# Kernel tuning notes

Measured on AMD Instinct MI355X. Metric: run time of the kernel, lower is better.

## Reference

```python
import jax, jax.numpy as jnp
import numpy as np

N_NODES = 50000
N_EDGES = 800000
IN_DIM = 128
HID_DIM = 256
OUT_DIM = 2


def setup_inputs() -> dict:
    key = jax.random.key(0)
    k = jax.random.split(key, 8)
    x = jax.random.normal(k[0], (N_NODES, IN_DIM), dtype=jnp.float32)
    edge_index = jax.random.randint(k[1], (2, N_EDGES), 0, N_NODES, dtype=jnp.int64)
    # Linear params (PyTorch-style fan-in scaling)
    W1 = jax.random.normal(k[2], (IN_DIM, HID_DIM), dtype=jnp.float32) / np.sqrt(IN_DIM)
    b1 = jnp.zeros((HID_DIM,), dtype=jnp.float32)
    W2 = jax.random.normal(k[3], (HID_DIM, OUT_DIM), dtype=jnp.float32) / np.sqrt(HID_DIM)
    b2 = jnp.zeros((OUT_DIM,), dtype=jnp.float32)
    # learnable GIN epsilons (init 0, as in PyG GINConv train_eps)
    eps1 = jnp.zeros((), dtype=jnp.float32)
    eps2 = jnp.zeros((), dtype=jnp.float32)
    return {"x": x, "edge_index": edge_index, "W1": W1, "b1": b1,
            "W2": W2, "b2": b2, "eps1": eps1, "eps2": eps2}


def _gin_conv(h, src, dst, num_nodes, eps, W, b):
    # aggregate: sum of neighbor features (scatter-add over edges)
    agg = jax.ops.segment_sum(h[src], dst, num_segments=num_nodes)  # [N, D]
    return ((1.0 + eps) * h + agg) @ W + b


def reference(x, edge_index, W1, b1, W2, b2, eps1, eps2):
    src, dst = edge_index[0], edge_index[1]
    n = x.shape[0]
    h = _gin_conv(x, src, dst, n, eps1, W1, b1)   # [N, HID]
    h = jax.nn.relu(h)
    out = _gin_conv(h, src, dst, n, eps2, W2, b2)  # [N, OUT]
    return out
```

## Files before the change

kernel.cpp:

```cpp
#include <hip/hip_runtime.h>

#define N_NODES 50000
#define N_EDGES 800000
#define IN_DIM 128
#define HID_DIM 256
#define OUT_DIM 2
#define CAP 64
#define NBKT 196
#define BCAP 6144
#define CHUNK 4096
#define POISON 0xAAAAAAAAu

typedef __attribute__((ext_vector_type(8))) short bh8;
typedef __attribute__((ext_vector_type(4))) float f4;
typedef __attribute__((ext_vector_type(4))) unsigned u4;

__device__ inline unsigned bf16rne(float f) {
    unsigned u = __float_as_uint(f);
    return (u + 0x7fffu + ((u >> 16) & 1u)) >> 16;
}
__device__ inline unsigned pack2(float lo, float hi) {
    return (bf16rne(hi) << 16) | bf16rne(lo);
}

__global__ __launch_bounds__(256) void k_prep_bin(
    const float* __restrict__ x, const float* __restrict__ W1,
    const int* __restrict__ ei,
    unsigned* __restrict__ xb, unsigned* __restrict__ W1p,
    unsigned* __restrict__ ccur, unsigned* __restrict__ coarse)
{
    __shared__ unsigned stage[CHUNK];
    __shared__ int hist[256], base[256], gpos[256], cur2[256];
    __shared__ int s_red[4];
    const int tid = threadIdx.x, lane = tid & 63, wv = tid >> 6;
    const int gtid = blockIdx.x * 256 + tid;
    const int gsz  = gridDim.x * 256;

    for (int i = gtid; i < 800000; i += gsz) {
        float4 a = ((const float4*)x)[2 * i];
        float4 b = ((const float4*)x)[2 * i + 1];
        u4 w;
        w[0] = pack2(a.x, a.y);
        w[1] = pack2(a.z, a.w);
        w[2] = pack2(b.x, b.y);
        w[3] = pack2(b.z, b.w);
        ((u4*)xb)[i] = w;
    }
    if (gtid < 16384) {
        int j = gtid;
        int d = j & 3, l = (j >> 2) & 63, s = (j >> 8) & 3, t = j >> 10;
        int k = 32 * s + 8 * (l >> 4) + 2 * d;
        int n = 16 * t + (l & 15);
        W1p[j] = (bf16rne(W1[(size_t)(k + 1) * HID_DIM + n]) << 16)
               |  bf16rne(W1[(size_t)k * HID_DIM + n]);
    }
    const int bid = blockIdx.x;
    if (bid >= NBKT) return;
    const int ebase = bid * CHUNK;
    const int ecnt  = min(CHUNK, N_EDGES - ebase);

    hist[tid] = 0;
    __syncthreads();
    int myd[16], mys[16];
#pragma unroll
    for (int r = 0; r < 16; r++) {
        int li = r * 256 + tid;
        if (li < ecnt) {
            int e = ebase + li;
            myd[r] = ei[N_EDGES + e];
            mys[r] = ei[e];
            atomicAdd(&hist[myd[r] >> 8], 1);
        } else myd[r] = -1;
    }
    __syncthreads();
    {
        int v = hist[tid], s = v;
#pragma unroll
        for (int off = 1; off < 64; off <<= 1) {
            int t = __shfl_up(s, off, 64);
            if (lane >= off) s += t;
        }
        if (lane == 63) s_red[wv] = s;
        __syncthreads();
        int wexcl = 0;
        for (int w = 0; w < wv; w++) wexcl += s_red[w];
        base[tid] = wexcl + s - v;
        cur2[tid] = 0;
        __syncthreads();
    }
    if (tid < NBKT && hist[tid] > 0) {
        atomicCAS(&ccur[tid], POISON, 0u);
        gpos[tid] = (int)atomicAdd(&ccur[tid], (unsigned)hist[tid]);
    }
    __syncthreads();
#pragma unroll
    for (int r = 0; r < 16; r++) {
        if (myd[r] >= 0) {
            int b = myd[r] >> 8;
            int pos = atomicAdd(&cur2[b], 1);
            stage[base[b] + pos] = ((unsigned)myd[r] << 16) | (unsigned)mys[r];
        }
    }
    __syncthreads();
    for (int i = tid; i < ecnt; i += 256) {
        unsigned rec = stage[i];
        int b = (int)(rec >> 24);
        int idx = gpos[b] + (i - base[b]);
        if (idx < BCAP) coarse[(size_t)b * BCAP + idx] = rec;
    }
}

__global__ __launch_bounds__(1024) void k_fine(
    const unsigned* __restrict__ ccur, const unsigned* __restrict__ coarse,
    int* __restrict__ slots, int* __restrict__ cnt)
{
    __shared__ int cur[256];
    const int tid = threadIdx.x, bid = blockIdx.x;
    if (tid < 256) cur[tid] = 0;
    __syncthreads();
    const int cb = min((int)ccur[bid], BCAP);
    unsigned recs[6];
#pragma unroll
    for (int r = 0; r < 6; r++) {
        int i = tid + r * 1024;
        if (i < cb) recs[r] = coarse[(size_t)bid * BCAP + i];
    }
#pragma unroll
    for (int r = 0; r < 6; r++) {
        int i = tid + r * 1024;
        if (i < cb) {
            unsigned rec = recs[r];
            int dst = (int)(rec >> 16);
            int src = (int)(rec & 0xffffu);
            int pos = atomicAdd(&cur[dst & 255], 1);
            if (pos < CAP) slots[(size_t)dst * CAP + pos] = src;
        }
    }
    __syncthreads();
    if (tid < 256) {
        int node = bid * 256 + tid;
        if (node < N_NODES) cnt[node] = min(cur[tid], CAP);
    }
}

__global__ __launch_bounds__(256, 4) void k_gin1(
    const unsigned* __restrict__ xb,
    const int* __restrict__ cnt, const int* __restrict__ slots,
    const unsigned* __restrict__ W1p, const float* __restrict__ b1,
    const float* __restrict__ W2, const float* __restrict__ b2,
    const float* __restrict__ eps1p, const float* __restrict__ eps2p,
    float* __restrict__ p, float* __restrict__ out)
{
    __shared__ __attribute__((aligned(16))) unsigned z[16 * 68];
    __shared__ float2 pp[64];
    const int tid = threadIdx.x, lane = tid & 63, wv = tid >> 6;
    const int node0 = blockIdx.x * 16;
    const int sub = lane & 15;
    const int grp = lane >> 4;
    const int node = node0 + 4 * wv + grp;
    const float e1 = 1.0f + eps1p[0];
    const u4* __restrict__ xb4 = (const u4*)xb;

    const int cn = min(cnt[node], CAP);
    const int4* srow = (const int4*)(slots + (size_t)node * CAP);
    int4 sg0 = srow[0], sg1 = srow[1], sg2 = srow[2], sg3 = srow[3];

    u4 us = xb4[(unsigned)(node * 16 + sub)];

    int sq[16];
    sq[0]=sg0.x;  sq[1]=sg0.y;  sq[2]=sg0.z;  sq[3]=sg0.w;
    sq[4]=sg1.x;  sq[5]=sg1.y;  sq[6]=sg1.z;  sq[7]=sg1.w;
    sq[8]=sg2.x;  sq[9]=sg2.y;  sq[10]=sg2.z; sq[11]=sg2.w;
    sq[12]=sg3.x; sq[13]=sg3.y; sq[14]=sg3.z; sq[15]=sg3.w;
#pragma unroll
    for (int g = 0; g < 16; g++) sq[g] = (g < cn) ? sq[g] : 0;

    u4 u[16];
#pragma unroll
    for (int g = 0; g < 16; g++)
        u[g] = xb4[(unsigned)(sq[g] * 16 + sub)];

    float ax[8];
#pragma unroll
    for (int k = 0; k < 8; k++) ax[k] = 0.f;
#pragma unroll
    for (int g = 0; g < 16; g++) {
        if (g < cn) {
#pragma unroll
            for (int k2 = 0; k2 < 4; k2++) {
                unsigned w = u[g][k2];
                ax[2 * k2]     += __uint_as_float(w << 16);
                ax[2 * k2 + 1] += __uint_as_float(w & 0xffff0000u);
            }
        }
    }
    int j0 = 16;
    while (__any(cn > j0)) {
        const int4* trow = (const int4*)(slots + (size_t)node * CAP + j0);
        int4 t0 = trow[0], t1 = trow[1], t2 = trow[2], t3 = trow[3];
        int tq[16];
        tq[0]=t0.x;  tq[1]=t0.y;  tq[2]=t0.z;  tq[3]=t0.w;
        tq[4]=t1.x;  tq[5]=t1.y;  tq[6]=t1.z;  tq[7]=t1.w;
        tq[8]=t2.x;  tq[9]=t2.y;  tq[10]=t2.z; tq[11]=t2.w;
        tq[12]=t3.x; tq[13]=t3.y; tq[14]=t3.z; tq[15]=t3.w;
#pragma unroll
        for (int g = 0; g < 16; g++) tq[g] = (j0 + g < cn) ? tq[g] : 0;
        u4 ut[16];
#pragma unroll
        for (int g = 0; g < 16; g++)
            ut[g] = xb4[(unsigned)(tq[g] * 16 + sub)];
#pragma unroll
        for (int g = 0; g < 16; g++) {
            if (j0 + g < cn) {
#pragma unroll
                for (int k2 = 0; k2 < 4; k2++) {
                    unsigned w = ut[g][k2];
                    ax[2 * k2]     += __uint_as_float(w << 16);
                    ax[2 * k2 + 1] += __uint_as_float(w & 0xffff0000u);
                }
            }
        }
        j0 += 16;
    }
    u4 zw;
#pragma unroll
    for (int k2 = 0; k2 < 4; k2++) {
        float lx = fmaf(e1, __uint_as_float(us[k2] << 16),         ax[2 * k2]);
        float ly = fmaf(e1, __uint_as_float(us[k2] & 0xffff0000u), ax[2 * k2 + 1]);
        zw[k2] = pack2(lx, ly);
    }
    *(u4*)&z[(4 * wv + grp) * 68 + 4 * sub] = zw;
    __syncthreads();

    const int q = lane >> 4, c = lane & 15;
    bh8 afrag[4];
#pragma unroll
    for (int s = 0; s < 4; s++)
        afrag[s] = *(const bh8*)&z[c * 68 + 16 * s + 4 * q];

    f4 acc[4];
#pragma unroll
    for (int t = 0; t < 4; t++) acc[t] = (f4){0.f, 0.f, 0.f, 0.f};
#pragma unroll
    for (int tp = 0; tp < 4; tp++) {
        int t = 4 * wv + tp;
#pragma unroll
        for (int s = 0; s < 4; s++) {
            bh8 bfrag = *(const bh8*)(W1p + ((size_t)(t * 4 + s) * 64 + lane) * 4);
            acc[tp] = __builtin_amdgcn_mfma_f32_16x16x32_bf16(afrag[s], bfrag, acc[tp], 0, 0, 0);
        }
    }

    const float e2 = 1.0f + eps2p[0];
    float pxr[4] = {0.f, 0.f, 0.f, 0.f};
    float pyr[4] = {0.f, 0.f, 0.f, 0.f};
#pragma unroll
    for (int tp = 0; tp < 4; tp++) {
        int n = 16 * (4 * wv + tp) + c;
        float bb = b1[n];
        float2 w2 = *(const float2*)(W2 + (size_t)n * OUT_DIM);
#pragma unroll
        for (int r = 0; r < 4; r++) {
            float h = fmaxf(acc[tp][r] + bb, 0.f);
            pxr[r] = fmaf(h, w2.x, pxr[r]);
            pyr[r] = fmaf(h, w2.y, pyr[r]);
        }
    }
#pragma unroll
    for (int off = 1; off < 16; off <<= 1) {
#pragma unroll
        for (int r = 0; r < 4; r++) {
            pxr[r] += __shfl_xor(pxr[r], off, 64);
            pyr[r] += __shfl_xor(pyr[r], off, 64);
        }
    }
    if (c == 0) {
#pragma unroll
        for (int r = 0; r < 4; r++)
            pp[wv * 16 + q * 4 + r] = make_float2(pxr[r], pyr[r]);
    }
    __syncthreads();

    if (tid < 16) {
        float px = 0.f, py = 0.f;
#pragma unroll
        for (int w = 0; w < 4; w++) {
            float2 v = pp[w * 16 + tid];
            px += v.x; py += v.y;
        }
        int nd = node0 + tid;
        *(float2*)(p + (size_t)nd * OUT_DIM) = make_float2(px, py);
        float2 b2v = *(const float2*)b2;
        float2 o;
        o.x = fmaf(e2, px, b2v.x);
        o.y = fmaf(e2, py, b2v.y);
        *(float2*)(out + (size_t)nd * OUT_DIM) = o;
    }
}

__global__ __launch_bounds__(256) void k_out(
    const int* __restrict__ cnt, const int* __restrict__ slots,
    const float* __restrict__ p, float* __restrict__ out)
{
    const int tid = threadIdx.x, lane = tid & 63, wv = tid >> 6;
    const int node = blockIdx.x * 32 + wv * 8 + (lane >> 3);
    const int l = lane & 7;
    float sx = 0.f, sy = 0.f;
    if (node < N_NODES) {
        int cn = min(cnt[node], CAP);
        const int4* srow = (const int4*)(slots + (size_t)node * CAP);
        for (int j0 = 0; j0 < cn; j0 += 32) {
            int4 s4 = srow[(j0 >> 2) + l];
            int jb = j0 + 4 * l;
            if (jb + 0 < cn) { float2 v = *(const float2*)(p + (size_t)s4.x * OUT_DIM); sx += v.x; sy += v.y; }
            if (jb + 1 < cn) { float2 v = *(const float2*)(p + (size_t)s4.y * OUT_DIM); sx += v.x; sy += v.y; }
            if (jb + 2 < cn) { float2 v = *(const float2*)(p + (size_t)s4.z * OUT_DIM); sx += v.x; sy += v.y; }
            if (jb + 3 < cn) { float2 v = *(const float2*)(p + (size_t)s4.w * OUT_DIM); sx += v.x; sy += v.y; }
        }
    }
#pragma unroll
    for (int off = 1; off <= 4; off <<= 1) {
        sx += __shfl_xor(sx, off, 64);
        sy += __shfl_xor(sy, off, 64);
    }
    if (l == 0 && node < N_NODES) {
        float2 o = *(const float2*)(out + (size_t)node * OUT_DIM);
        o.x += sx; o.y += sy;
        *(float2*)(out + (size_t)node * OUT_DIM) = o;
    }
}

extern "C" void kernel_launch(void* const* d_in, const int* in_sizes, int n_in,
                              void* d_out, int out_size, void* d_ws, size_t ws_size,
                              hipStream_t stream)
{
    (void)in_sizes; (void)n_in; (void)out_size; (void)ws_size;
    const float* x    = (const float*)d_in[0];
    const int*   ei   = (const int*)d_in[1];
    const float* W1   = (const float*)d_in[2];
    const float* b1   = (const float*)d_in[3];
    const float* W2   = (const float*)d_in[4];
    const float* b2   = (const float*)d_in[5];
    const float* eps1 = (const float*)d_in[6];
    const float* eps2 = (const float*)d_in[7];
    float* out = (float*)d_out;

    int* cnt         = (int*)d_ws;
    int* slots       = cnt + 50048;
    float* p         = (float*)(slots + 3200000);
    unsigned* xb     = (unsigned*)(p + 100000);
    unsigned* W1p    = xb + 3200000;
    unsigned* ccur   = (unsigned*)(W1p + 16384);
    unsigned* coarse = ccur + 256;

    k_prep_bin<<<2048, 256, 0, stream>>>(x, W1, ei, xb, W1p, ccur, coarse);
    k_fine<<<NBKT, 1024, 0, stream>>>(ccur, coarse, slots, cnt);
    k_gin1<<<(N_NODES + 15) / 16, 256, 0, stream>>>(xb, cnt, slots,
                                                    W1p, b1, W2, b2,
                                                    eps1, eps2, p, out);
    k_out<<<(N_NODES + 31) / 32, 256, 0, stream>>>(cnt, slots, p, out);
}
```

Before: 152.1 us.

## Gather half of neighbor rows via direct global-to-LDS loads and split prep blocks

```diff
diff --git a/kernel.cpp b/kernel.cpp
--- a/kernel.cpp
+++ b/kernel.cpp
@@ -33,29 +33,32 @@
     __shared__ int hist[256], base[256], gpos[256], cur2[256];
     __shared__ int s_red[4];
     const int tid = threadIdx.x, lane = tid & 63, wv = tid >> 6;
-    const int gtid = blockIdx.x * 256 + tid;
-    const int gsz  = gridDim.x * 256;
-
-    for (int i = gtid; i < 800000; i += gsz) {
-        float4 a = ((const float4*)x)[2 * i];
-        float4 b = ((const float4*)x)[2 * i + 1];
-        u4 w;
-        w[0] = pack2(a.x, a.y);
-        w[1] = pack2(a.z, a.w);
-        w[2] = pack2(b.x, b.y);
-        w[3] = pack2(b.z, b.w);
-        ((u4*)xb)[i] = w;
-    }
-    if (gtid < 16384) {
-        int j = gtid;
-        int d = j & 3, l = (j >> 2) & 63, s = (j >> 8) & 3, t = j >> 10;
-        int k = 32 * s + 8 * (l >> 4) + 2 * d;
-        int n = 16 * t + (l & 15);
-        W1p[j] = (bf16rne(W1[(size_t)(k + 1) * HID_DIM + n]) << 16)
-               |  bf16rne(W1[(size_t)k * HID_DIM + n]);
-    }
     const int bid = blockIdx.x;
-    if (bid >= NBKT) return;
+
+    if (bid >= NBKT) {
+        const int gt = (bid - NBKT) * 256 + tid;
+        const int gs = ((int)gridDim.x - NBKT) * 256;
+        for (int i = gt; i < 800000; i += gs) {
+            float4 a = ((const float4*)x)[2 * i];
+            float4 b = ((const float4*)x)[2 * i + 1];
+            u4 w;
+            w[0] = pack2(a.x, a.y);
+            w[1] = pack2(a.z, a.w);
+            w[2] = pack2(b.x, b.y);
+            w[3] = pack2(b.z, b.w);
+            ((u4*)xb)[i] = w;
+        }
+        if (gt < 16384) {
+            int j = gt;
+            int d = j & 3, l = (j >> 2) & 63, s = (j >> 8) & 3, t = j >> 10;
+            int k = 32 * s + 8 * (l >> 4) + 2 * d;
+            int n = 16 * t + (l & 15);
+            W1p[j] = (bf16rne(W1[(size_t)(k + 1) * HID_DIM + n]) << 16)
+                   |  bf16rne(W1[(size_t)k * HID_DIM + n]);
+        }
+        return;
+    }
+
     const int ebase = bid * CHUNK;
     const int ecnt  = min(CHUNK, N_EDGES - ebase);
 
@@ -139,7 +142,12 @@
     __syncthreads();
     if (tid < 256) {
         int node = bid * 256 + tid;
-        if (node < N_NODES) cnt[node] = min(cur[tid], CAP);
+        if (node < N_NODES) {
+            int cn = min(cur[tid], CAP);
+            cnt[node] = cn;
+            for (int j = cn; j < 16; j++)
+                slots[(size_t)node * CAP + j] = 0;
+        }
     }
 }
 
@@ -151,6 +159,7 @@
     const float* __restrict__ eps1p, const float* __restrict__ eps2p,
     float* __restrict__ p, float* __restrict__ out)
 {
+    __shared__ __attribute__((aligned(16))) unsigned gbuf[4][8][256];
     __shared__ __attribute__((aligned(16))) unsigned z[16 * 68];
     __shared__ float2 pp[64];
     const int tid = threadIdx.x, lane = tid & 63, wv = tid >> 6;
@@ -164,7 +173,6 @@
     const int cn = min(cnt[node], CAP);
     const int4* srow = (const int4*)(slots + (size_t)node * CAP);
     int4 sg0 = srow[0], sg1 = srow[1], sg2 = srow[2], sg3 = srow[3];
-
     u4 us = xb4[(unsigned)(node * 16 + sub)];
 
     int sq[16];
@@ -172,23 +180,44 @@
     sq[4]=sg1.x;  sq[5]=sg1.y;  sq[6]=sg1.z;  sq[7]=sg1.w;
     sq[8]=sg2.x;  sq[9]=sg2.y;  sq[10]=sg2.z; sq[11]=sg2.w;
     sq[12]=sg3.x; sq[13]=sg3.y; sq[14]=sg3.z; sq[15]=sg3.w;
-#pragma unroll
-    for (int g = 0; g < 16; g++) sq[g] = (g < cn) ? sq[g] : 0;
-
-    u4 u[16];
-#pragma unroll
-    for (int g = 0; g < 16; g++)
-        u[g] = xb4[(unsigned)(sq[g] * 16 + sub)];
+
+#pragma unroll
+    for (int g = 0; g < 8; g++) {
+        const unsigned* gp = xb + (size_t)((unsigned)sq[g]) * 64 + 4 * sub;
+        __builtin_amdgcn_global_load_lds(
+            (const __attribute__((address_space(1))) void*)gp,
+            (__attribute__((address_space(3))) void*)(&gbuf[wv][g][0]),
+            16, 0, 0);
+    }
+    u4 u[8];
+#pragma unroll
+    for (int g = 0; g < 8; g++)
+        u[g] = xb4[(unsigned)((unsigned)sq[8 + g] * 16 + sub)];
 
     float ax[8];
 #pragma unroll
     for (int k = 0; k < 8; k++) ax[k] = 0.f;
-#pragma unroll
-    for (int g = 0; g < 16; g++) {
-        if (g < cn) {
+
+    asm volatile("s_waitcnt vmcnt(0)" ::: "memory");
+
+#pragma unroll
+    for (int g = 0; g < 8; g++) {
+        if (8 + g < cn) {
 #pragma unroll
             for (int k2 = 0; k2 < 4; k2++) {
                 unsigned w = u[g][k2];
+                ax[2 * k2]     += __uint_as_float(w << 16);
+                ax[2 * k2 + 1] += __uint_as_float(w & 0xffff0000u);
+            }
+        }
+    }
+#pragma unroll
+    for (int g = 0; g < 8; g++) {
+        if (g < cn) {
+            u4 w4 = *(const u4*)&gbuf[wv][g][4 * lane];
+#pragma unroll
+            for (int k2 = 0; k2 < 4; k2++) {
+                unsigned w = w4[k2];
                 ax[2 * k2]     += __uint_as_float(w << 16);
                 ax[2 * k2 + 1] += __uint_as_float(w & 0xffff0000u);
             }
@@ -208,7 +237,7 @@
         u4 ut[16];
 #pragma unroll
         for (int g = 0; g < 16; g++)
-            ut[g] = xb4[(unsigned)(tq[g] * 16 + sub)];
+            ut[g] = xb4[(unsigned)((unsigned)tq[g] * 16 + sub)];
 #pragma unroll
         for (int g = 0; g < 16; g++) {
             if (j0 + g < cn) {
```

Result: no change. 152.9 us (+0.6%).

## Replace two-pass LDS-binned adjacency build with direct global atomic scatter

Applied to the files above, without the earlier changes.

```diff
diff --git a/kernel.cpp b/kernel.cpp
--- a/kernel.cpp
+++ b/kernel.cpp
@@ -6,9 +6,6 @@
 #define HID_DIM 256
 #define OUT_DIM 2
 #define CAP 64
-#define NBKT 196
-#define BCAP 6144
-#define CHUNK 4096
 #define POISON 0xAAAAAAAAu
 
 typedef __attribute__((ext_vector_type(8))) short bh8;
@@ -23,18 +20,15 @@
     return (bf16rne(hi) << 16) | bf16rne(lo);
 }
 
-__global__ __launch_bounds__(256) void k_prep_bin(
+__global__ __launch_bounds__(256) void k_prep(
     const float* __restrict__ x, const float* __restrict__ W1,
-    const int* __restrict__ ei,
     unsigned* __restrict__ xb, unsigned* __restrict__ W1p,
-    unsigned* __restrict__ ccur, unsigned* __restrict__ coarse)
-{
-    __shared__ unsigned stage[CHUNK];
-    __shared__ int hist[256], base[256], gpos[256], cur2[256];
-    __shared__ int s_red[4];
-    const int tid = threadIdx.x, lane = tid & 63, wv = tid >> 6;
-    const int gtid = blockIdx.x * 256 + tid;
+    int* __restrict__ cnt)
+{
+    const int gtid = blockIdx.x * 256 + threadIdx.x;
     const int gsz  = gridDim.x * 256;
+
+    if (gtid < 50048) cnt[gtid] = 0;
 
     for (int i = gtid; i < 800000; i += gsz) {
         float4 a = ((const float4*)x)[2 * i];
@@ -54,93 +48,23 @@
         W1p[j] = (bf16rne(W1[(size_t)(k + 1) * HID_DIM + n]) << 16)
                |  bf16rne(W1[(size_t)k * HID_DIM + n]);
     }
-    const int bid = blockIdx.x;
-    if (bid >= NBKT) return;
-    const int ebase = bid * CHUNK;
-    const int ecnt  = min(CHUNK, N_EDGES - ebase);
-
-    hist[tid] = 0;
-    __syncthreads();
-    int myd[16], mys[16];
-#pragma unroll
-    for (int r = 0; r < 16; r++) {
-        int li = r * 256 + tid;
-        if (li < ecnt) {
-            int e = ebase + li;
-            myd[r] = ei[N_EDGES + e];
-            mys[r] = ei[e];
-            atomicAdd(&hist[myd[r] >> 8], 1);
-        } else myd[r] = -1;
-    }
-    __syncthreads();
-    {
-        int v = hist[tid], s = v;
-#pragma unroll
-        for (int off = 1; off < 64; off <<= 1) {
-            int t = __shfl_up(s, off, 64);
-            if (lane >= off) s += t;
-        }
-        if (lane == 63) s_red[wv] = s;
-        __syncthreads();
-        int wexcl = 0;
-        for (int w = 0; w < wv; w++) wexcl += s_red[w];
-        base[tid] = wexcl + s - v;
-        cur2[tid] = 0;
-        __syncthreads();
-    }
-    if (tid < NBKT && hist[tid] > 0) {
-        atomicCAS(&ccur[tid], POISON, 0u);
-        gpos[tid] = (int)atomicAdd(&ccur[tid], (unsigned)hist[tid]);
-    }
-    __syncthreads();
-#pragma unroll
-    for (int r = 0; r < 16; r++) {
-        if (myd[r] >= 0) {
-            int b = myd[r] >> 8;
-            int pos = atomicAdd(&cur2[b], 1);
-            stage[base[b] + pos] = ((unsigned)myd[r] << 16) | (unsigned)mys[r];
-        }
-    }
-    __syncthreads();
-    for (int i = tid; i < ecnt; i += 256) {
-        unsigned rec = stage[i];
-        int b = (int)(rec >> 24);
-        int idx = gpos[b] + (i - base[b]);
-        if (idx < BCAP) coarse[(size_t)b * BCAP + idx] = rec;
-    }
-}
-
-__global__ __launch_bounds__(1024) void k_fine(
-    const unsigned* __restrict__ ccur, const unsigned* __restrict__ coarse,
-    int* __restrict__ slots, int* __restrict__ cnt)
-{
-    __shared__ int cur[256];
-    const int tid = threadIdx.x, bid = blockIdx.x;
-    if (tid < 256) cur[tid] = 0;
-    __syncthreads();
-    const int cb = min((int)ccur[bid], BCAP);
-    unsigned recs[6];
-#pragma unroll
-    for (int r = 0; r < 6; r++) {
-        int i = tid + r * 1024;
-        if (i < cb) recs[r] = coarse[(size_t)bid * BCAP + i];
-    }
-#pragma unroll
-    for (int r = 0; r < 6; r++) {
-        int i = tid + r * 1024;
-        if (i < cb) {
-            unsigned rec = recs[r];
-            int dst = (int)(rec >> 16);
-            int src = (int)(rec & 0xffffu);
-            int pos = atomicAdd(&cur[dst & 255], 1);
-            if (pos < CAP) slots[(size_t)dst * CAP + pos] = src;
-        }
-    }
-    __syncthreads();
-    if (tid < 256) {
-        int node = bid * 256 + tid;
-        if (node < N_NODES) cnt[node] = min(cur[tid], CAP);
-    }
+}
+
+__global__ __launch_bounds__(256) void k_scat(
+    const int* __restrict__ ei, int* __restrict__ cnt, int* __restrict__ slots)
+{
+    const int t = blockIdx.x * 256 + threadIdx.x;
+    if (t >= N_EDGES / 4) return;
+    int4 s4 = ((const int4*)ei)[t];
+    int4 d4 = ((const int4*)(ei + N_EDGES))[t];
+    int p0 = atomicAdd(&cnt[d4.x], 1);
+    if (p0 < CAP) slots[(size_t)d4.x * CAP + p0] = s4.x;
+    int p1 = atomicAdd(&cnt[d4.y], 1);
+    if (p1 < CAP) slots[(size_t)d4.y * CAP + p1] = s4.y;
+    int p2 = atomicAdd(&cnt[d4.z], 1);
+    if (p2 < CAP) slots[(size_t)d4.z * CAP + p2] = s4.z;
+    int p3 = atomicAdd(&cnt[d4.w], 1);
+    if (p3 < CAP) slots[(size_t)d4.w * CAP + p3] = s4.w;
 }
 
 __global__ __launch_bounds__(256, 4) void k_gin1(
@@ -208,7 +132,7 @@
         u4 ut[16];
 #pragma unroll
         for (int g = 0; g < 16; g++)
-            ut[g] = xb4[(unsigned)(tq[g] * 16 + sub)];
+            ut[g] = xb4[(unsigned)((unsigned)tq[g] * 16 + sub)];
 #pragma unroll
         for (int g = 0; g < 16; g++) {
             if (j0 + g < cn) {
@@ -350,11 +274,9 @@
     float* p         = (float*)(slots + 3200000);
     unsigned* xb     = (unsigned*)(p + 100000);
     unsigned* W1p    = xb + 3200000;
-    unsigned* ccur   = (unsigned*)(W1p + 16384);
-    unsigned* coarse = ccur + 256;
-
-    k_prep_bin<<<2048, 256, 0, stream>>>(x, W1, ei, xb, W1p, ccur, coarse);
-    k_fine<<<NBKT, 1024, 0, stream>>>(ccur, coarse, slots, cnt);
+
+    k_prep<<<2048, 256, 0, stream>>>(x, W1, xb, W1p, cnt);
+    k_scat<<<(N_EDGES / 4 + 255) / 256, 256, 0, stream>>>(ei, cnt, slots);
     k_gin1<<<(N_NODES + 15) / 16, 256, 0, stream>>>(xb, cnt, slots,
                                                     W1p, b1, W2, b2,
                                                     eps1, eps2, p, out);
```

Result: slower. 178.8 us (+17.6%).
